# Kernel tuning notes

Measured on AMD Instinct MI355X. Metric: run time of the kernel, lower is better.

The kernel has to match this reference:

```python
import jax, jax.numpy as jnp
import numpy as np
import math

B, T, D = 2, 2048, 1024
H, DH = 16, 64          # num_heads, head_dim
DFF = 4096              # 4*d_model
EPS = 1e-5


def _layernorm(x, g, b):
    m = jnp.mean(x, axis=-1, keepdims=True)
    v = jnp.mean(jnp.square(x - m), axis=-1, keepdims=True)
    return (x - m) * jax.lax.rsqrt(v + EPS) * g + b


def setup_inputs() -> dict:
    key = jax.random.key(0)
    ks = jax.random.split(key, 6)
    s = 0.02
    return {
        "x": jax.random.normal(ks[0], (B, T, D), dtype=jnp.float32),
        "ln1_g": jnp.ones((D,), jnp.float32), "ln1_b": jnp.zeros((D,), jnp.float32),
        "ln2_g": jnp.ones((D,), jnp.float32), "ln2_b": jnp.zeros((D,), jnp.float32),
        "w_qkv": jax.random.normal(ks[1], (3 * D, D), jnp.float32) * s,
        "b_qkv": jnp.zeros((3 * D,), jnp.float32),
        "w_out": jax.random.normal(ks[2], (D, D), jnp.float32) * s,
        "b_out": jnp.zeros((D,), jnp.float32),
        "w1": jax.random.normal(ks[3], (DFF, D), jnp.float32) * s,
        "b1": jnp.zeros((DFF,), jnp.float32),
        "w2": jax.random.normal(ks[4], (D, DFF), jnp.float32) * s,
        "b2": jnp.zeros((D,), jnp.float32),
    }


def reference(x, ln1_g, ln1_b, ln2_g, ln2_b, w_qkv, b_qkv, w_out, b_out, w1, b1, w2, b2):
    # --- attention sublayer (Pre-LN) ---
    h = _layernorm(x, ln1_g, ln1_b)                       # [B,T,D]
    qkv = h @ w_qkv.T + b_qkv                             # [B,T,3D]
    qkv = qkv.reshape(B, T, 3, H, DH).transpose(2, 0, 3, 1, 4)  # [3,B,H,T,DH]
    q, k, v = qkv[0], qkv[1], qkv[2]
    scores = jnp.einsum('bhqd,bhkd->bhqk', q, k) / math.sqrt(DH)  # [B,H,T,T]
    causal = jnp.tril(jnp.ones((T, T), dtype=bool))
    scores = jnp.where(causal, scores, -jnp.inf)
    weights = jax.nn.softmax(scores, axis=-1)
    attn = jnp.einsum('bhqk,bhkd->bhqd', weights, v)      # [B,H,T,DH]
    attn = attn.transpose(0, 2, 1, 3).reshape(B, T, D)
    x = x + (attn @ w_out.T + b_out)

    # --- FFN sublayer (Pre-LN, exact GELU) ---
    h2 = _layernorm(x, ln2_g, ln2_b)
    ff = jax.nn.gelu(h2 @ w1.T + b1, approximate=False) @ w2.T + b2
    return x + ff
```

## Files before the change

kernel.cpp:

```cpp
#include <hip/hip_runtime.h>
#include <hip/hip_bf16.h>
#include <cmath>

typedef __bf16 bf16x8 __attribute__((ext_vector_type(8)));
typedef float  f32x4  __attribute__((ext_vector_type(4)));

#define LDS_AS __attribute__((address_space(3)))
#define GLB_AS __attribute__((address_space(1)))

__device__ __forceinline__ void gll16(const void* g, void* l) {
    __builtin_amdgcn_global_load_lds((const GLB_AS unsigned int*)g,
                                     (LDS_AS unsigned int*)l, 16, 0, 0);
}

__device__ __forceinline__ f32x4 mfma16(bf16x8 a, bf16x8 b, f32x4 c) {
    return __builtin_amdgcn_mfma_f32_16x16x32_bf16(a, b, c, 0, 0, 0);
}

__device__ __forceinline__ unsigned short f2bf(float f) {
    __hip_bfloat16 b = __float2bfloat16(f);
    return *reinterpret_cast<unsigned short*>(&b);
}

__device__ __forceinline__ bf16x8 swzfrag(const __hip_bfloat16* __restrict__ lds,
                                          int row, int cb)
{
    const int addr = row * 128 + (cb ^ ((row & 7) << 4));
    return *(const bf16x8*)((const char*)lds + addr);
}

__device__ __forceinline__ void stage64x128B(const char* __restrict__ base, int pitch,
                                             char* __restrict__ lds, int t)
{
#pragma unroll
    for (int i = 0; i < 2; ++i) {
        const int d   = i * 4096 + t * 16;
        const int row = d >> 7;
        const int x   = d & 127;
        const int gx  = x ^ ((row & 7) << 4);
        gll16(base + (size_t)row * pitch + gx, lds + d);
    }
}

__device__ __forceinline__ void stage128x128B(const char* __restrict__ base, int pitch,
                                              char* __restrict__ lds, int t)
{
#pragma unroll
    for (int i = 0; i < 4; ++i) {
        const int d   = i * 4096 + t * 16;
        const int row = d >> 7;
        const int x   = d & 127;
        const int gx  = x ^ ((row & 7) << 4);
        gll16(base + (size_t)row * pitch + gx, lds + d);
    }
}

#define TB   2
#define TT   2048
#define TD   1024
#define TH   16
#define TDH  64
#define TDFF 4096
#define TM   4096

__global__ __launch_bounds__(256)
void cvt_kernel(const float* __restrict__ src, __hip_bfloat16* __restrict__ dst, int n4)
{
    int i = blockIdx.x * 256 + threadIdx.x;
    if (i >= n4) return;
    float4 v = ((const float4*)src)[i];
    ushort4 o;
    o.x = f2bf(v.x); o.y = f2bf(v.y); o.z = f2bf(v.z); o.w = f2bf(v.w);
    ((ushort4*)dst)[i] = o;
}

__global__ __launch_bounds__(256)
void ln_kernel(const float* __restrict__ x, const float* __restrict__ g,
               const float* __restrict__ b, __hip_bfloat16* __restrict__ out)
{
    const int row = blockIdx.x;
    const int t = threadIdx.x;
    const float4 v = *(const float4*)(x + (size_t)row * TD + t * 4);
    float s  = v.x + v.y + v.z + v.w;
    float ss = v.x*v.x + v.y*v.y + v.z*v.z + v.w*v.w;
#pragma unroll
    for (int d = 1; d < 64; d <<= 1) { s += __shfl_xor(s, d); ss += __shfl_xor(ss, d); }
    __shared__ float red[8];
    const int wv = t >> 6, lane = t & 63;
    if (lane == 0) { red[wv] = s; red[4 + wv] = ss; }
    __syncthreads();
    s  = red[0] + red[1] + red[2] + red[3];
    ss = red[4] + red[5] + red[6] + red[7];
    const float mean = s * (1.0f / TD);
    const float var  = ss * (1.0f / TD) - mean * mean;
    const float rstd = rsqrtf(var + 1e-5f);
    const float4 gv = *(const float4*)(g + t * 4);
    const float4 bv = *(const float4*)(b + t * 4);
    ushort4 o;
    o.x = f2bf((v.x - mean) * rstd * gv.x + bv.x);
    o.y = f2bf((v.y - mean) * rstd * gv.y + bv.y);
    o.z = f2bf((v.z - mean) * rstd * gv.z + bv.z);
    o.w = f2bf((v.w - mean) * rstd * gv.w + bv.w);
    *(ushort4*)(out + (size_t)row * TD + t * 4) = o;
}

template<int EPI>
__global__ __launch_bounds__(512)
void gemm_dual(const __hip_bfloat16* __restrict__ A, const __hip_bfloat16* __restrict__ Bw,
               const float* __restrict__ bias,
               __hip_bfloat16* __restrict__ outb,
               __hip_bfloat16* __restrict__ qb, __hip_bfloat16* __restrict__ kb,
               __hip_bfloat16* __restrict__ vtb,
               int M, int N, int K)
{
    __shared__ char ldsraw[131072];
    const int t = threadIdx.x;
    const int tl = t & 255;
    const int lane = t & 63, w = t >> 6;
    const int grp = w >> 2;
    const int wl = w & 3;
    const int wr = wl >> 1, wc = wl & 1;
    const int l15 = lane & 15, lg = lane >> 4;
    const int bn = blockIdx.x, bm = blockIdx.y;

    f32x4 acc[4][4] = {};

    const char* Ab = (const char*)(A  + (size_t)(bm * 256 + grp * 128) * K);
    const char* Bb = (const char*)(Bw + (size_t)bn * 128 * K);
    const int pitch = K * 2;
    char* base = ldsraw + grp * 65536;

    const int nt = K >> 6;
    stage128x128B(Ab, pitch, base, tl);
    stage128x128B(Bb, pitch, base + 32768, tl);

    for (int it = 0; it < nt; ++it) {
        const int cb = (it & 1) * 16384;
        if (it + 1 < nt) {
            const size_t koff = (size_t)(it + 1) * 128;
            const int nb = ((it + 1) & 1) * 16384;
            stage128x128B(Ab + koff, pitch, base + nb, tl);
            stage128x128B(Bb + koff, pitch, base + 32768 + nb, tl);
            asm volatile("s_waitcnt vmcnt(8)" ::: "memory");
        } else {
            asm volatile("s_waitcnt vmcnt(0)" ::: "memory");
        }
        __builtin_amdgcn_s_barrier();
        __builtin_amdgcn_sched_barrier(0);
        const __hip_bfloat16* bufA = (const __hip_bfloat16*)(base + cb);
        const __hip_bfloat16* bufB = (const __hip_bfloat16*)(base + 32768 + cb);
        bf16x8 af[4][2], bfr[4][2];
#pragma unroll
        for (int mf = 0; mf < 4; ++mf)
#pragma unroll
            for (int kk = 0; kk < 2; ++kk)
                af[mf][kk] = swzfrag(bufA, wr * 64 + mf * 16 + l15, kk * 64 + lg * 16);
#pragma unroll
        for (int nf = 0; nf < 4; ++nf)
#pragma unroll
            for (int kk = 0; kk < 2; ++kk)
                bfr[nf][kk] = swzfrag(bufB, wc * 64 + nf * 16 + l15, kk * 64 + lg * 16);
        __builtin_amdgcn_s_setprio(1);
#pragma unroll
        for (int mf = 0; mf < 4; ++mf)
#pragma unroll
            for (int nf = 0; nf < 4; ++nf) {
                acc[mf][nf] = mfma16(af[mf][0], bfr[nf][0], acc[mf][nf]);
                acc[mf][nf] = mfma16(af[mf][1], bfr[nf][1], acc[mf][nf]);
            }
        __builtin_amdgcn_s_setprio(0);
        __builtin_amdgcn_s_barrier();
    }

#pragma unroll
    for (int mf = 0; mf < 4; ++mf) {
#pragma unroll
        for (int nf = 0; nf < 4; ++nf) {
#pragma unroll
            for (int r = 0; r < 4; ++r) {
                const int mg = bm * 256 + grp * 128 + wr * 64 + mf * 16 + lg * 4 + r;
                const int ng = bn * 128 + wc * 64 + nf * 16 + l15;
                const float v = acc[mf][nf][r] + bias[ng];
                if constexpr (EPI == 2) {
                    const float ge = 0.5f * v * (1.0f + erff(v * 0.70710678118654752f));
                    outb[(size_t)mg * N + ng] = __float2bfloat16(ge);
                } else {
                    const int which = ng >> 10;
                    const int hh = (ng >> 6) & 15;
                    const int dh = ng & 63;
                    const int bb = mg >> 11;
                    const int tt2 = mg & 2047;
                    const int bhid = bb * TH + hh;
                    const __hip_bfloat16 bv = __float2bfloat16(v);
                    if (which == 0)      qb[((size_t)bhid * TT + tt2) * TDH + dh] = bv;
                    else if (which == 1) kb[((size_t)bhid * TT + tt2) * TDH + dh] = bv;
                    else                 vtb[((size_t)bhid * TDH + dh) * TT + tt2] = bv;
                }
            }
        }
    }
}

__global__ __launch_bounds__(512)
void gemm_sk(const __hip_bfloat16* __restrict__ A, const __hip_bfloat16* __restrict__ Bw,
             const float* __restrict__ bias, const float* __restrict__ resid,
             float* __restrict__ outf, int M, int N, int K)
{
    __shared__ char ldsraw[131072];
    const int t = threadIdx.x;
    const int tl = t & 255;
    const int lane = t & 63, w = t >> 6;
    const int grp = w >> 2;
    const int wl = w & 3;
    const int wr = wl >> 1, wc = wl & 1;
    const int l15 = lane & 15, lg = lane >> 4;
    const int bn = blockIdx.x, bm = blockIdx.y;

    f32x4 acc[4][4] = {};

    const int Kh = K >> 1;
    const char* Ab = (const char*)(A  + (size_t)bm * 128 * K) + (size_t)grp * Kh * 2;
    const char* Bb = (const char*)(Bw + (size_t)bn * 128 * K) + (size_t)grp * Kh * 2;
    const int pitch = K * 2;
    char* base = ldsraw + grp * 65536;

    const int nt = Kh >> 6;
    stage128x128B(Ab, pitch, base, tl);
    stage128x128B(Bb, pitch, base + 32768, tl);

    for (int it = 0; it < nt; ++it) {
        const int cb = (it & 1) * 16384;
        if (it + 1 < nt) {
            const size_t koff = (size_t)(it + 1) * 128;
            const int nb = ((it + 1) & 1) * 16384;
            stage128x128B(Ab + koff, pitch, base + nb, tl);
            stage128x128B(Bb + koff, pitch, base + 32768 + nb, tl);
            asm volatile("s_waitcnt vmcnt(8)" ::: "memory");
        } else {
            asm volatile("s_waitcnt vmcnt(0)" ::: "memory");
        }
        __builtin_amdgcn_s_barrier();
        __builtin_amdgcn_sched_barrier(0);
        const __hip_bfloat16* bufA = (const __hip_bfloat16*)(base + cb);
        const __hip_bfloat16* bufB = (const __hip_bfloat16*)(base + 32768 + cb);
        bf16x8 af[4][2], bfr[4][2];
#pragma unroll
        for (int mf = 0; mf < 4; ++mf)
#pragma unroll
            for (int kk = 0; kk < 2; ++kk)
                af[mf][kk] = swzfrag(bufA, wr * 64 + mf * 16 + l15, kk * 64 + lg * 16);
#pragma unroll
        for (int nf = 0; nf < 4; ++nf)
#pragma unroll
            for (int kk = 0; kk < 2; ++kk)
                bfr[nf][kk] = swzfrag(bufB, wc * 64 + nf * 16 + l15, kk * 64 + lg * 16);
        __builtin_amdgcn_s_setprio(1);
#pragma unroll
        for (int mf = 0; mf < 4; ++mf)
#pragma unroll
            for (int nf = 0; nf < 4; ++nf) {
                acc[mf][nf] = mfma16(af[mf][0], bfr[nf][0], acc[mf][nf]);
                acc[mf][nf] = mfma16(af[mf][1], bfr[nf][1], acc[mf][nf]);
            }
        __builtin_amdgcn_s_setprio(0);
        __builtin_amdgcn_s_barrier();
    }

    float* xch = (float*)ldsraw;
    if (grp == 1) {
#pragma unroll
        for (int mf = 0; mf < 4; ++mf)
#pragma unroll
            for (int nf = 0; nf < 4; ++nf)
#pragma unroll
                for (int r = 0; r < 4; ++r)
                    xch[(wr * 64 + mf * 16 + lg * 4 + r) * 132 + wc * 64 + nf * 16 + l15] =
                        acc[mf][nf][r];
    }
    __syncthreads();
    if (grp == 0) {
#pragma unroll
        for (int mf = 0; mf < 4; ++mf)
#pragma unroll
            for (int nf = 0; nf < 4; ++nf)
#pragma unroll
                for (int r = 0; r < 4; ++r) {
                    const int mgl = wr * 64 + mf * 16 + lg * 4 + r;
                    const int ngl = wc * 64 + nf * 16 + l15;
                    const int mg = bm * 128 + mgl;
                    const int ng = bn * 128 + ngl;
                    const size_t o = (size_t)mg * N + ng;
                    outf[o] = acc[mf][nf][r] + xch[mgl * 132 + ngl] + bias[ng] + resid[o];
                }
    }
}

__global__ __launch_bounds__(256)
void flash_kernel(const __hip_bfloat16* __restrict__ q, const __hip_bfloat16* __restrict__ k,
                  const __hip_bfloat16* __restrict__ vt, __hip_bfloat16* __restrict__ attn)
{
    const int L  = blockIdx.y * gridDim.x + blockIdx.x;
    const int cu = L & 255;
    const int s  = L >> 8;
    const int q0 = cu & 31;
    const int qt = (s & 1) ? (31 - q0) : q0;
    const int bh = s * 8 + (cu >> 5);

    const int t = threadIdx.x;
    const int w = t >> 6, lane = t & 63;
    const int l15 = lane & 15, lg = lane >> 4;
    const int qrow0 = qt * 64 + w * 16;
    const __hip_bfloat16* Qb = q  + (size_t)bh * TT * TDH;
    const __hip_bfloat16* Kb = k  + (size_t)bh * TT * TDH;
    const __hip_bfloat16* Vb = vt + (size_t)bh * TDH * TT;

    __shared__ __hip_bfloat16 kt[2][64 * 64];
    __shared__ __hip_bfloat16 vtt[2][64 * 64];
    __shared__ __hip_bfloat16 plds[4][16 * 64];

    bf16x8 qa[2];
#pragma unroll
    for (int c = 0; c < 2; ++c)
        qa[c] = *(const bf16x8*)(Qb + (size_t)(qrow0 + l15) * TDH + c * 32 + lg * 8);

    f32x4 o[4] = {};
    float mrun = -INFINITY, lrun = 0.0f;

    const int nt = qt + 1;
    int cur = 0;
    stage64x128B((const char*)Kb, 128, (char*)kt[0], t);
    stage64x128B((const char*)Vb, TT * 2, (char*)vtt[0], t);
    __syncthreads();

    for (int it = 0; it < nt; ++it) {
        const int kv0 = it * 64;
        if (it + 1 < nt) {
            stage64x128B((const char*)Kb + (size_t)(kv0 + 64) * 128, 128, (char*)kt[cur ^ 1], t);
            stage64x128B((const char*)Vb + (size_t)(kv0 + 64) * 2, TT * 2, (char*)vtt[cur ^ 1], t);
        }
        f32x4 sc[4] = {};
#pragma unroll
        for (int j = 0; j < 4; ++j) {
            const bf16x8 kb0 = swzfrag(kt[cur], j * 16 + l15, lg * 16);
            const bf16x8 kb1 = swzfrag(kt[cur], j * 16 + l15, 64 + lg * 16);
            sc[j] = mfma16(kb0, qa[0], sc[j]);
            sc[j] = mfma16(kb1, qa[1], sc[j]);
        }
        if (it == nt - 1) {
            const int qg = qrow0 + l15;
#pragma unroll
            for (int j = 0; j < 4; ++j)
#pragma unroll
                for (int r = 0; r < 4; ++r) {
                    const int kvg = kv0 + j * 16 + lg * 4 + r;
                    sc[j][r] = (kvg <= qg) ? sc[j][r] * 0.125f : -INFINITY;
                }
        } else {
#pragma unroll
            for (int j = 0; j < 4; ++j)
#pragma unroll
                for (int r = 0; r < 4; ++r) sc[j][r] *= 0.125f;
        }
        float pm;
        {
            float m0 = fmaxf(fmaxf(sc[0][0], sc[0][1]), fmaxf(sc[0][2], sc[0][3]));
            float m1 = fmaxf(fmaxf(sc[1][0], sc[1][1]), fmaxf(sc[1][2], sc[1][3]));
            float m2 = fmaxf(fmaxf(sc[2][0], sc[2][1]), fmaxf(sc[2][2], sc[2][3]));
            float m3 = fmaxf(fmaxf(sc[3][0], sc[3][1]), fmaxf(sc[3][2], sc[3][3]));
            pm = fmaxf(fmaxf(m0, m1), fmaxf(m2, m3));
        }
        pm = fmaxf(pm, __shfl_xor(pm, 16));
        pm = fmaxf(pm, __shfl_xor(pm, 32));

        const float mn = fmaxf(mrun, pm);
        const float alpha = __expf(mrun - mn);
        mrun = mn;
        f32x4 p[4];
        float rs = 0.0f;
#pragma unroll
        for (int j = 0; j < 4; ++j) {
            float a = 0.0f;
#pragma unroll
            for (int r = 0; r < 4; ++r) { p[j][r] = __expf(sc[j][r] - mn); a += p[j][r]; }
            rs += a;
        }
        rs += __shfl_xor(rs, 16);
        rs += __shfl_xor(rs, 32);
        lrun = lrun * alpha + rs;
#pragma unroll
        for (int nf = 0; nf < 4; ++nf)
#pragma unroll
            for (int r = 0; r < 4; ++r) o[nf][r] *= alpha;
        {
            __hip_bfloat16* pw = plds[w];
#pragma unroll
            for (int j = 0; j < 4; ++j) {
                ushort4 pk;
                pk.x = f2bf(p[j][0]); pk.y = f2bf(p[j][1]);
                pk.z = f2bf(p[j][2]); pk.w = f2bf(p[j][3]);
                const int cb = j * 32 + lg * 8;
                *(ushort4*)((char*)pw + l15 * 128 + (cb ^ ((l15 & 7) << 4))) = pk;
            }
        }
        asm volatile("s_waitcnt lgkmcnt(0)" ::: "memory");
        __builtin_amdgcn_sched_barrier(0);
        bf16x8 pb[2];
#pragma unroll
        for (int c = 0; c < 2; ++c)
            pb[c] = swzfrag(plds[w], l15, c * 64 + lg * 16);
#pragma unroll
        for (int nf = 0; nf < 4; ++nf) {
            const bf16x8 vb0 = swzfrag(vtt[cur], nf * 16 + l15, lg * 16);
            const bf16x8 vb1 = swzfrag(vtt[cur], nf * 16 + l15, 64 + lg * 16);
            o[nf] = mfma16(vb0, pb[0], o[nf]);
            o[nf] = mfma16(vb1, pb[1], o[nf]);
        }
        __syncthreads();
        cur ^= 1;
    }

    const int bb = bh >> 4, hh = bh & 15;
    const float inv = 1.0f / lrun;
    const int tt = qrow0 + l15;
#pragma unroll
    for (int nf = 0; nf < 4; ++nf) {
        const int d0 = nf * 16 + lg * 4;
        ushort4 st;
        st.x = f2bf(o[nf][0] * inv);
        st.y = f2bf(o[nf][1] * inv);
        st.z = f2bf(o[nf][2] * inv);
        st.w = f2bf(o[nf][3] * inv);
        *(ushort4*)(attn + ((size_t)(bb * TT + tt)) * TD + hh * TDH + d0) = st;
    }
}

extern "C" void kernel_launch(void* const* d_in, const int* in_sizes, int n_in,
                              void* d_out, int out_size, void* d_ws, size_t ws_size,
                              hipStream_t stream)
{
    const float* x     = (const float*)d_in[0];
    const float* ln1_g = (const float*)d_in[1];
    const float* ln1_b = (const float*)d_in[2];
    const float* ln2_g = (const float*)d_in[3];
    const float* ln2_b = (const float*)d_in[4];
    const float* w_qkv = (const float*)d_in[5];
    const float* b_qkv = (const float*)d_in[6];
    const float* w_out = (const float*)d_in[7];
    const float* b_out = (const float*)d_in[8];
    const float* w1    = (const float*)d_in[9];
    const float* b1    = (const float*)d_in[10];
    const float* w2    = (const float*)d_in[11];
    const float* b2    = (const float*)d_in[12];

    char* ws = (char*)d_ws;
    __hip_bfloat16* wqkv_bf = (__hip_bfloat16*)(ws + 0);
    __hip_bfloat16* wout_bf = (__hip_bfloat16*)(ws + 6291456);
    __hip_bfloat16* w1_bf   = (__hip_bfloat16*)(ws + 8388608);
    __hip_bfloat16* w2_bf   = (__hip_bfloat16*)(ws + 16777216);
    float*          x2      = (float*)(ws + 25165824);
    __hip_bfloat16* hbuf    = (__hip_bfloat16*)(ws + 41943040);
    __hip_bfloat16* qbuf    = (__hip_bfloat16*)(ws + 50331648);
    __hip_bfloat16* kbuf    = (__hip_bfloat16*)(ws + 58720256);
    __hip_bfloat16* vtbuf   = (__hip_bfloat16*)(ws + 67108864);
    __hip_bfloat16* attnbuf = (__hip_bfloat16*)(ws + 75497472);
    __hip_bfloat16* ff1     = (__hip_bfloat16*)(ws + 50331648);

    cvt_kernel<<<3072, 256, 0, stream>>>(w_qkv, wqkv_bf, 3 * TD * TD / 4);
    cvt_kernel<<<1024, 256, 0, stream>>>(w_out, wout_bf, TD * TD / 4);
    cvt_kernel<<<4096, 256, 0, stream>>>(w1, w1_bf, TDFF * TD / 4);
    cvt_kernel<<<4096, 256, 0, stream>>>(w2, w2_bf, TD * TDFF / 4);

    ln_kernel<<<TM, 256, 0, stream>>>(x, ln1_g, ln1_b, hbuf);
    gemm_dual<0><<<dim3(24, 16), 512, 0, stream>>>(hbuf, wqkv_bf, b_qkv,
                                                   nullptr, qbuf, kbuf, vtbuf,
                                                   TM, 3 * TD, TD);
    flash_kernel<<<dim3(32, 32), 256, 0, stream>>>(qbuf, kbuf, vtbuf, attnbuf);
    gemm_sk<<<dim3(8, 32), 512, 0, stream>>>(attnbuf, wout_bf, b_out, x,
                                             x2, TM, TD, TD);
    ln_kernel<<<TM, 256, 0, stream>>>(x2, ln2_g, ln2_b, hbuf);
    gemm_dual<2><<<dim3(32, 16), 512, 0, stream>>>(hbuf, w1_bf, b1,
                                                   ff1, nullptr, nullptr, nullptr,
                                                   TM, TDFF, TD);
    gemm_sk<<<dim3(8, 32), 512, 0, stream>>>(ff1, w2_bf, b2, x2,
                                             (float*)d_out, TM, TD, TDFF);
}
```

Baseline: 260.9 us.

## Replace dual-group GEMM with 256-thread BK=32 kernel using small LDS footprint

The QKV and FFN1 GEMMs previously ran 512-thread blocks with two 128-row groups sharing a 128KB LDS allocation and K-step 64. They now use 256-thread blocks computing a 128x128 tile with K-step 32, a new swizzle for 64-byte rows, and only 32KB of LDS. The grid doubles in the M direction. The aim is higher occupancy with more resident blocks per CU, at the cost of twice as many barriers per K and some loss of operand reuse across the two groups. The flash kernel also raises wave priority around its MFMA sections.

Result: faster. 248.9 us (-4.6%).

```diff
diff --git a/kernel.cpp b/kernel.cpp
--- a/kernel.cpp
+++ b/kernel.cpp
@@ -27,6 +27,30 @@
 {
     const int addr = row * 128 + (cb ^ ((row & 7) << 4));
     return *(const bf16x8*)((const char*)lds + addr);
+}
+
+__device__ __forceinline__ bf16x8 swzfrag32(const __hip_bfloat16* __restrict__ lds,
+                                            int row, int cb)
+{
+    const int L = row >> 1;
+    const int s = ((row & 1) << 2) | (cb >> 4);
+    const int addr = (L << 7) | (((s ^ (L & 7)) << 4) | (cb & 15));
+    return *(const bf16x8*)((const char*)lds + addr);
+}
+
+__device__ __forceinline__ void stage128x64B_swz(const char* __restrict__ base, int pitch,
+                                                 char* __restrict__ lds, int t)
+{
+#pragma unroll
+    for (int i = 0; i < 2; ++i) {
+        const int d  = i * 4096 + t * 16;
+        const int L  = d >> 7;
+        const int sp = (d >> 4) & 7;
+        const int s  = sp ^ (L & 7);
+        const int r  = (L << 1) | (s >> 2);
+        const int gx = (s & 3) << 4;
+        gll16(base + (size_t)r * pitch + gx, lds + d);
+    }
 }
 
 __device__ __forceinline__ void stage64x128B(const char* __restrict__ base, int pitch,
@@ -105,69 +129,58 @@
 }
 
 template<int EPI>
-__global__ __launch_bounds__(512)
-void gemm_dual(const __hip_bfloat16* __restrict__ A, const __hip_bfloat16* __restrict__ Bw,
+__global__ __launch_bounds__(256)
+void gemm_bt32(const __hip_bfloat16* __restrict__ A, const __hip_bfloat16* __restrict__ Bw,
                const float* __restrict__ bias,
                __hip_bfloat16* __restrict__ outb,
                __hip_bfloat16* __restrict__ qb, __hip_bfloat16* __restrict__ kb,
                __hip_bfloat16* __restrict__ vtb,
                int M, int N, int K)
 {
-    __shared__ char ldsraw[131072];
+    __shared__ __hip_bfloat16 ldsA[2][128 * 32];
+    __shared__ __hip_bfloat16 ldsB[2][128 * 32];
     const int t = threadIdx.x;
-    const int tl = t & 255;
-    const int lane = t & 63, w = t >> 6;
-    const int grp = w >> 2;
-    const int wl = w & 3;
-    const int wr = wl >> 1, wc = wl & 1;
+    const int lane = t & 63, wv = t >> 6;
+    const int wr = wv >> 1, wc = wv & 1;
     const int l15 = lane & 15, lg = lane >> 4;
     const int bn = blockIdx.x, bm = blockIdx.y;
 
     f32x4 acc[4][4] = {};
 
-    const char* Ab = (const char*)(A  + (size_t)(bm * 256 + grp * 128) * K);
+    const char* Ab = (const char*)(A  + (size_t)bm * 128 * K);
     const char* Bb = (const char*)(Bw + (size_t)bn * 128 * K);
     const int pitch = K * 2;
-    char* base = ldsraw + grp * 65536;
-
-    const int nt = K >> 6;
-    stage128x128B(Ab, pitch, base, tl);
-    stage128x128B(Bb, pitch, base + 32768, tl);
+
+    const int nt = K >> 5;
+    stage128x64B_swz(Ab, pitch, (char*)ldsA[0], t);
+    stage128x64B_swz(Bb, pitch, (char*)ldsB[0], t);
 
     for (int it = 0; it < nt; ++it) {
-        const int cb = (it & 1) * 16384;
         if (it + 1 < nt) {
-            const size_t koff = (size_t)(it + 1) * 128;
-            const int nb = ((it + 1) & 1) * 16384;
-            stage128x128B(Ab + koff, pitch, base + nb, tl);
-            stage128x128B(Bb + koff, pitch, base + 32768 + nb, tl);
-            asm volatile("s_waitcnt vmcnt(8)" ::: "memory");
+            const size_t koff = (size_t)(it + 1) * 64;
+            stage128x64B_swz(Ab + koff, pitch, (char*)ldsA[(it + 1) & 1], t);
+            stage128x64B_swz(Bb + koff, pitch, (char*)ldsB[(it + 1) & 1], t);
+            asm volatile("s_waitcnt vmcnt(4)" ::: "memory");
         } else {
             asm volatile("s_waitcnt vmcnt(0)" ::: "memory");
         }
         __builtin_amdgcn_s_barrier();
         __builtin_amdgcn_sched_barrier(0);
-        const __hip_bfloat16* bufA = (const __hip_bfloat16*)(base + cb);
-        const __hip_bfloat16* bufB = (const __hip_bfloat16*)(base + 32768 + cb);
-        bf16x8 af[4][2], bfr[4][2];
+        const __hip_bfloat16* bufA = ldsA[it & 1];
+        const __hip_bfloat16* bufB = ldsB[it & 1];
+        bf16x8 af[4], bfr[4];
 #pragma unroll
         for (int mf = 0; mf < 4; ++mf)
-#pragma unroll
-            for (int kk = 0; kk < 2; ++kk)
-                af[mf][kk] = swzfrag(bufA, wr * 64 + mf * 16 + l15, kk * 64 + lg * 16);
+            af[mf] = swzfrag32(bufA, wr * 64 + mf * 16 + l15, lg * 16);
 #pragma unroll
         for (int nf = 0; nf < 4; ++nf)
-#pragma unroll
-            for (int kk = 0; kk < 2; ++kk)
-                bfr[nf][kk] = swzfrag(bufB, wc * 64 + nf * 16 + l15, kk * 64 + lg * 16);
+            bfr[nf] = swzfrag32(bufB, wc * 64 + nf * 16 + l15, lg * 16);
         __builtin_amdgcn_s_setprio(1);
 #pragma unroll
         for (int mf = 0; mf < 4; ++mf)
 #pragma unroll
-            for (int nf = 0; nf < 4; ++nf) {
-                acc[mf][nf] = mfma16(af[mf][0], bfr[nf][0], acc[mf][nf]);
-                acc[mf][nf] = mfma16(af[mf][1], bfr[nf][1], acc[mf][nf]);
-            }
+            for (int nf = 0; nf < 4; ++nf)
+                acc[mf][nf] = mfma16(af[mf], bfr[nf], acc[mf][nf]);
         __builtin_amdgcn_s_setprio(0);
         __builtin_amdgcn_s_barrier();
     }
@@ -178,7 +191,7 @@
         for (int nf = 0; nf < 4; ++nf) {
 #pragma unroll
             for (int r = 0; r < 4; ++r) {
-                const int mg = bm * 256 + grp * 128 + wr * 64 + mf * 16 + lg * 4 + r;
+                const int mg = bm * 128 + wr * 64 + mf * 16 + lg * 4 + r;
                 const int ng = bn * 128 + wc * 64 + nf * 16 + l15;
                 const float v = acc[mf][nf][r] + bias[ng];
                 if constexpr (EPI == 2) {
@@ -339,6 +352,7 @@
             stage64x128B((const char*)Vb + (size_t)(kv0 + 64) * 2, TT * 2, (char*)vtt[cur ^ 1], t);
         }
         f32x4 sc[4] = {};
+        __builtin_amdgcn_s_setprio(1);
 #pragma unroll
         for (int j = 0; j < 4; ++j) {
             const bf16x8 kb0 = swzfrag(kt[cur], j * 16 + l15, lg * 16);
@@ -346,6 +360,7 @@
             sc[j] = mfma16(kb0, qa[0], sc[j]);
             sc[j] = mfma16(kb1, qa[1], sc[j]);
         }
+        __builtin_amdgcn_s_setprio(0);
         if (it == nt - 1) {
             const int qg = qrow0 + l15;
 #pragma unroll
@@ -408,6 +423,7 @@
 #pragma unroll
         for (int c = 0; c < 2; ++c)
             pb[c] = swzfrag(plds[w], l15, c * 64 + lg * 16);
+        __builtin_amdgcn_s_setprio(1);
 #pragma unroll
         for (int nf = 0; nf < 4; ++nf) {
             const bf16x8 vb0 = swzfrag(vtt[cur], nf * 16 + l15, lg * 16);
@@ -415,6 +431,7 @@
             o[nf] = mfma16(vb0, pb[0], o[nf]);
             o[nf] = mfma16(vb1, pb[1], o[nf]);
         }
+        __builtin_amdgcn_s_setprio(0);
         __syncthreads();
         cur ^= 1;
     }
@@ -471,14 +488,14 @@
     cvt_kernel<<<4096, 256, 0, stream>>>(w2, w2_bf, TD * TDFF / 4);
 
     ln_kernel<<<TM, 256, 0, stream>>>(x, ln1_g, ln1_b, hbuf);
-    gemm_dual<0><<<dim3(24, 16), 512, 0, stream>>>(hbuf, wqkv_bf, b_qkv,
+    gemm_bt32<0><<<dim3(24, 32), 256, 0, stream>>>(hbuf, wqkv_bf, b_qkv,
                                                    nullptr, qbuf, kbuf, vtbuf,
                                                    TM, 3 * TD, TD);
     flash_kernel<<<dim3(32, 32), 256, 0, stream>>>(qbuf, kbuf, vtbuf, attnbuf);
     gemm_sk<<<dim3(8, 32), 512, 0, stream>>>(attnbuf, wout_bf, b_out, x,
                                              x2, TM, TD, TD);
     ln_kernel<<<TM, 256, 0, stream>>>(x2, ln2_g, ln2_b, hbuf);
-    gemm_dual<2><<<dim3(32, 16), 512, 0, stream>>>(hbuf, w1_bf, b1,
+    gemm_bt32<2><<<dim3(32, 32), 256, 0, stream>>>(hbuf, w1_bf, b1,
                                                    ff1, nullptr, nullptr, nullptr,
                                                    TM, TDFF, TD);
     gemm_sk<<<dim3(8, 32), 512, 0, stream>>>(ff1, w2_bf, b2, x2,
```
